# Optimization experiments

Measured on AMD Instinct MI355X. Metric: run time of the kernel, lower is better.

Reference implementation:

```python
import jax, jax.numpy as jnp
import numpy as np

B, N, D_IN, D_OUT, D_EDGE = 2, 512, 128, 128, 32
NEG_SLOPE = 0.2  # GATv2 LeakyReLU default


def _glorot(k, shape):
    lim = np.sqrt(6.0 / (shape[0] + shape[1]))
    return jax.random.uniform(k, shape, jnp.float32, -lim, lim)


def setup_inputs() -> dict:
    key = jax.random.key(0)
    ks = jax.random.split(key, 8)
    return {
        "node_features": jax.random.normal(ks[0], (B, N, D_IN), jnp.float32),
        "adj": jax.random.uniform(ks[1], (B, N, N)) < 0.1,  # sparse-ish dense adjacency
        "edge_features": jax.random.normal(ks[2], (B, N, N, D_EDGE), jnp.float32),
        "mask": jnp.ones((B, N), dtype=bool),
        "W_l": _glorot(ks[3], (D_IN, D_OUT)),   # source (lin_l)
        "b_l": jnp.zeros((D_OUT,), jnp.float32),
        "W_r": _glorot(ks[4], (D_IN, D_OUT)),   # target (lin_r)
        "b_r": jnp.zeros((D_OUT,), jnp.float32),
        "W_e": _glorot(ks[5], (D_EDGE, D_OUT)), # lin_edge (no bias)
        "att": _glorot(ks[6], (1, D_OUT))[0],   # attention vector [D_OUT]
        "bias": jnp.zeros((D_OUT,), jnp.float32),
    }


def _gatv2_dense(x, adj, e, mask, W_l, b_l, W_r, b_r, W_e, att, bias):
    # add self-loops (dense GAT convention)
    adj = adj | jnp.eye(N, dtype=bool)
    x_l = x @ W_l + b_l              # [B,N,D] source transform
    x_r = x @ W_r + b_r              # [B,N,D] target transform
    e_t = e @ W_e                    # [B,N,N,D] edge transform
    # edge (j -> i): pre[b,i,j,:] = x_l[b,j] + x_r[b,i] + e_t[b,i,j]
    pre = x_l[:, None, :, :] + x_r[:, :, None, :] + e_t
    score = jnp.einsum('bijd,d->bij', jax.nn.leaky_relu(pre, NEG_SLOPE), att)
    score = jnp.where(adj, score, -jnp.inf)
    alpha = jax.nn.softmax(score, axis=-1)  # softmax over neighbors j
    out = jnp.einsum('bij,bjd->bid', alpha, x_l) + bias
    return jnp.where(mask[:, :, None], out, 0.0)


def reference(node_features, adj, edge_features, mask, W_l, b_l, W_r, b_r, W_e, att, bias):
    return jax.nn.silu(
        _gatv2_dense(node_features, adj, edge_features, mask,
                     W_l, b_l, W_r, b_r, W_e, att, bias)
    )
```

## Files before the change

### kernel.cpp

```cpp
#include <hip/hip_runtime.h>
#include <math.h>

#define BATCH 2
#define NNODE 512
#define DIN   128
#define DOUT  128
#define DE    32
#define NEG   0.2f
#define TI    4
#define TJ    64
#define TIB   4

typedef __attribute__((ext_vector_type(8))) short bf16x8;
typedef __attribute__((ext_vector_type(4))) float f32x4;

__device__ inline short f2bf(float f) {
    union { float f; unsigned u; } v; v.f = f;
    unsigned r = v.u + 0x7fffu + ((v.u >> 16) & 1u);
    return (short)(r >> 16);
}

template<int CTRL>
__device__ inline float dpp_add(float x) {
    const int y = __builtin_amdgcn_update_dpp(0, __float_as_int(x), CTRL, 0xF, 0xF, false);
    return x + __int_as_float(y);
}
__device__ inline float row16_sum(float x) {
    x = dpp_add<0x128>(x);
    x = dpp_add<0x124>(x);
    x = dpp_add<0x122>(x);
    x = dpp_add<0x121>(x);
    return x;
}

__global__ __launch_bounds__(256) void xlr_kernel(
    const float* __restrict__ x,  const float* __restrict__ Wl,
    const float* __restrict__ bl, const float* __restrict__ Wr,
    const float* __restrict__ br, float* __restrict__ xl,
    float* __restrict__ xr)
{
    const int r0 = blockIdx.x * 4;
    const int d  = threadIdx.x & 127;
    const int hv = threadIdx.x >> 7;
    __shared__ float xs[4][DIN];
    for (int idx = threadIdx.x; idx < 4 * DIN; idx += 256)
        xs[idx >> 7][idx & 127] = x[(size_t)r0 * DIN + idx];
    __syncthreads();
    const int ra = 2 * hv, rb = ra + 1;
    float al0 = bl[d], al1 = al0, ar0 = br[d], ar1 = ar0;
    #pragma unroll 4
    for (int k = 0; k < DIN; ++k) {
        const float wl = Wl[k * DOUT + d], wr = Wr[k * DOUT + d];
        const float xa = xs[ra][k], xb = xs[rb][k];
        al0 = fmaf(xa, wl, al0); al1 = fmaf(xb, wl, al1);
        ar0 = fmaf(xa, wr, ar0); ar1 = fmaf(xb, wr, ar1);
    }
    xl[(size_t)(r0 + ra) * DOUT + d] = al0;
    xl[(size_t)(r0 + rb) * DOUT + d] = al1;
    xr[(size_t)(r0 + ra) * DOUT + d] = ar0;
    xr[(size_t)(r0 + rb) * DOUT + d] = ar1;
}

__global__ __launch_bounds__(256, 4) void score_kernel(
    const float* __restrict__ xl, const float* __restrict__ xr,
    const float* __restrict__ e,  const float* __restrict__ We,
    const float* __restrict__ att, float* __restrict__ sc)
{
    const int bid = blockIdx.x;
    const int jT  = bid & 7;
    const int iT  = (bid >> 3) & 127;
    const int b   = bid >> 10;
    const int i0  = iT * TI, j0 = jT * TJ;
    const int t    = threadIdx.x;
    const int wave = t >> 6;
    const int lane = t & 63;
    const int col  = lane & 15;
    const int g    = lane >> 4;

    __shared__ short WeT_s[DOUT][DE];
    __shared__ float xr_s[TI][DOUT];
    __shared__ float att_s[DOUT];

    for (int idx = t; idx < DE * DOUT; idx += 256) {
        const int k = idx >> 7, d = idx & 127;
        WeT_s[d][k] = f2bf(We[idx]);
    }
    for (int idx = t; idx < TI * DOUT; idx += 256) {
        const int ii = idx >> 7, d = idx & 127;
        xr_s[ii][d] = xr[(size_t)(b * NNODE + i0 + ii) * DOUT + d];
    }
    if (t < DOUT) att_s[t] = att[t];

    f32x4 xlv4[8];
    {
        const float* xb = xl + (size_t)(b * NNODE + j0 + wave * 16 + g * 4) * DOUT + col;
        #pragma unroll
        for (int dt = 0; dt < 8; ++dt)
            #pragma unroll
            for (int r = 0; r < 4; ++r)
                xlv4[dt][r] = xb[(size_t)r * DOUT + dt * 16];
    }
    __syncthreads();

    bf16x8 bf[8];
    float  atv[8];
    #pragma unroll
    for (int dt = 0; dt < 8; ++dt) {
        bf[dt]  = *(const bf16x8*)&WeT_s[dt * 16 + col][g * 8];
        atv[dt] = att_s[dt * 16 + col];
    }

    const int jw = j0 + wave * 16;
    const float* ebase = e + ((size_t)(b * NNODE + i0) * NNODE + jw + col) * DE + g * 8;
    const size_t estep = (size_t)NNODE * DE;

    f32x4 a0 = *(const f32x4*)ebase;
    f32x4 a1 = *(const f32x4*)(ebase + 4);

    for (int i = 0; i < TI; ++i) {
        f32x4 a0n, a1n;
        if (i + 1 < TI) {
            const float* apn = ebase + (size_t)(i + 1) * estep;
            a0n = *(const f32x4*)apn;
            a1n = *(const f32x4*)(apn + 4);
        }
        bf16x8 af;
        af[0] = f2bf(a0[0]); af[1] = f2bf(a0[1]);
        af[2] = f2bf(a0[2]); af[3] = f2bf(a0[3]);
        af[4] = f2bf(a1[0]); af[5] = f2bf(a1[1]);
        af[6] = f2bf(a1[2]); af[7] = f2bf(a1[3]);

        float part[4] = {0.f, 0.f, 0.f, 0.f};
        #pragma unroll
        for (int dt = 0; dt < 8; ++dt) {
            const f32x4 c = __builtin_amdgcn_mfma_f32_16x16x32_bf16(af, bf[dt], xlv4[dt], 0, 0, 0);
            const float xrv = xr_s[i][dt * 16 + col];
            #pragma unroll
            for (int r = 0; r < 4; ++r) {
                float p = c[r] + xrv;
                p = fmaxf(p, NEG * p);
                part[r] = fmaf(atv[dt], p, part[r]);
            }
        }
        #pragma unroll
        for (int r = 0; r < 4; ++r)
            part[r] = row16_sum(part[r]);

        if (col == 0) {
            float4 v;
            float* vp = (float*)&v;
            #pragma unroll
            for (int r = 0; r < 4; ++r) vp[r] = part[r];
            *(float4*)&sc[(size_t)(b * NNODE + i0 + i) * NNODE + jw + g * 4] = v;
        }
        a0 = a0n; a1 = a1n;
    }
}

__global__ __launch_bounds__(256) void agg_kernel(
    const float* __restrict__ xl, const float* __restrict__ sc,
    const void* __restrict__ adjv, const void* __restrict__ maskv,
    const float* __restrict__ bias, float* __restrict__ out)
{
    const int bid = blockIdx.x;
    const int dh  = bid & 1;
    const int iT  = (bid >> 1) & 127;
    const int b   = bid >> 8;
    const int i0  = iT * TIB, d0 = dh * 64;
    const int t    = threadIdx.x;
    const int wave = t >> 6;
    const int lane = t & 63;

    __shared__ float al_s[TIB][NNODE];
    __shared__ float ps_s[4][TIB][64];
    __shared__ float inv_s[TIB];
    __shared__ int   mflag[2];

    if (t < 2) mflag[t] = 0;
    {
        const unsigned* aw = (const unsigned*)adjv;
        unsigned sawF = 0, sawG = 0;
        #pragma unroll
        for (int k = 0; k < 16; ++k) {
            const unsigned w = aw[t + 256 * k];
            sawF |= (w == 0x3f800000u);
            sawG |= (w > 1u);
        }
        if (sawF) atomicOr(&mflag[0], 1);
        if (sawG) atomicOr(&mflag[1], 1);
    }
    for (int idx = t; idx < TIB * NNODE; idx += 256) {
        const int r = idx >> 9, jj = idx & 511;
        al_s[r][jj] = sc[(size_t)(b * NNODE + i0 + r) * NNODE + jj];
    }
    __syncthreads();
    const int byteMode = (!mflag[0] && mflag[1]) ? 1 : 0;

    {
        const int ig = i0 + wave;
        const unsigned char* aB = (const unsigned char*)adjv + (size_t)(b * NNODE + ig) * NNODE;
        const unsigned*      aW = (const unsigned*)adjv + (size_t)(b * NNODE + ig) * NNODE;
        float v[8], m = -1e30f;
        #pragma unroll
        for (int k = 0; k < 8; ++k) {
            const int j = lane + 64 * k;
            const bool conn = (j == ig) ||
                (byteMode ? (aB[j] != 0) : (aW[j] != 0));
            v[k] = conn ? al_s[wave][j] : -1e30f;
            m = fmaxf(m, v[k]);
        }
        #pragma unroll
        for (int off = 32; off; off >>= 1) m = fmaxf(m, __shfl_xor(m, off, 64));
        float s = 0.f;
        #pragma unroll
        for (int k = 0; k < 8; ++k) {
            const float ex = __expf(v[k] - m);
            al_s[wave][lane + 64 * k] = ex;
            s += ex;
        }
        #pragma unroll
        for (int off = 32; off; off >>= 1) s += __shfl_xor(s, off, 64);
        if (lane == 0) inv_s[wave] = 1.f / s;
    }
    __syncthreads();

    const int d = d0 + lane;
    const float* xb = xl + (size_t)b * NNODE * DOUT + d;
    float ac[TIB] = {0.f, 0.f, 0.f, 0.f};
    const int jlo = wave * 128;
    for (int j4 = jlo; j4 < jlo + 128; j4 += 4) {
        const f32x4 a0 = *(const f32x4*)&al_s[0][j4];
        const f32x4 a1 = *(const f32x4*)&al_s[1][j4];
        const f32x4 a2 = *(const f32x4*)&al_s[2][j4];
        const f32x4 a3 = *(const f32x4*)&al_s[3][j4];
        #pragma unroll
        for (int k = 0; k < 4; ++k) {
            const float xv = xb[(size_t)(j4 + k) * DOUT];
            ac[0] = fmaf(a0[k], xv, ac[0]);
            ac[1] = fmaf(a1[k], xv, ac[1]);
            ac[2] = fmaf(a2[k], xv, ac[2]);
            ac[3] = fmaf(a3[k], xv, ac[3]);
        }
    }
    #pragma unroll
    for (int r = 0; r < TIB; ++r) ps_s[wave][r][lane] = ac[r];
    __syncthreads();

    {
        const int r = wave;
        float val = (ps_s[0][r][lane] + ps_s[1][r][lane]) +
                    (ps_s[2][r][lane] + ps_s[3][r][lane]);
        const int mi = b * NNODE + i0 + r;
        const bool mv = byteMode ? (((const unsigned char*)maskv)[mi] != 0)
                                 : (((const unsigned*)maskv)[mi] != 0);
        val = val * inv_s[r] + bias[d];
        if (!mv) val = 0.f;
        val = val / (1.f + __expf(-val));
        out[(size_t)mi * DOUT + d] = val;
    }
}

extern "C" void kernel_launch(void* const* d_in, const int* in_sizes, int n_in,
                              void* d_out, int out_size, void* d_ws, size_t ws_size,
                              hipStream_t stream)
{
    const float* x    = (const float*)d_in[0];
    const void*  adj  = d_in[1];
    const float* e    = (const float*)d_in[2];
    const void*  mask = d_in[3];
    const float* Wl   = (const float*)d_in[4];
    const float* bl   = (const float*)d_in[5];
    const float* Wr   = (const float*)d_in[6];
    const float* br   = (const float*)d_in[7];
    const float* We   = (const float*)d_in[8];
    const float* att  = (const float*)d_in[9];
    const float* bias = (const float*)d_in[10];
    float*       out  = (float*)d_out;

    float* xl = (float*)d_ws;
    float* xr = xl + (size_t)BATCH * NNODE * DOUT;
    float* sc = xr + (size_t)BATCH * NNODE * DOUT;

    xlr_kernel<<<(BATCH * NNODE) / 4, 256, 0, stream>>>(x, Wl, bl, Wr, br, xl, xr);
    score_kernel<<<BATCH * (NNODE / TI) * (NNODE / TJ), 256, 0, stream>>>(
        xl, xr, e, We, att, sc);
    agg_kernel<<<BATCH * (NNODE / TIB) * 2, 256, 0, stream>>>(
        xl, sc, adj, mask, bias, out);
}
```

Measured before the change: 51.43 us.

## Stage edge tiles through LDS with async global_load_lds triple buffering

The score kernel now streams each edge-feature row tile into a swizzled three-slot LDS ring using direct global-to-LDS loads, keeping two rows in flight while the current one is computed. It also doubles the rows per block (TI 4→8), uses packed bf16 conversion instructions, and stages scores in LDS so they leave in coalesced float4 stores. The aim is to hide the memory latency of the dominant 64MB edge tensor read and to cut conversion ALU work. In exchange it adds about 24KB of LDS per block, a barrier per row, and halves the number of blocks, which can lower occupancy.

```diff
diff --git a/kernel.cpp b/kernel.cpp
--- a/kernel.cpp
+++ b/kernel.cpp
@@ -7,7 +7,7 @@
 #define DOUT  128
 #define DE    32
 #define NEG   0.2f
-#define TI    4
+#define TI    8
 #define TJ    64
 #define TIB   4
 
@@ -18,6 +18,19 @@
     union { float f; unsigned u; } v; v.f = f;
     unsigned r = v.u + 0x7fffu + ((v.u >> 16) & 1u);
     return (short)(r >> 16);
+}
+
+__device__ inline unsigned cvtpk(float lo, float hi) {
+    unsigned r;
+    asm("v_cvt_pk_bf16_f32 %0, %1, %2" : "=v"(r) : "v"(lo), "v"(hi));
+    return r;
+}
+typedef union { bf16x8 v; unsigned u[4]; } bfu;
+
+__device__ inline void gload16(const void* g, void* l) {
+    __builtin_amdgcn_global_load_lds(
+        (const __attribute__((address_space(1))) void*)g,
+        (__attribute__((address_space(3))) void*)l, 16, 0, 0);
 }
 
 template<int CTRL>
@@ -61,15 +74,15 @@
     xr[(size_t)(r0 + rb) * DOUT + d] = ar1;
 }
 
-__global__ __launch_bounds__(256, 4) void score_kernel(
+__global__ __launch_bounds__(256, 2) void score_kernel(
     const float* __restrict__ xl, const float* __restrict__ xr,
     const float* __restrict__ e,  const float* __restrict__ We,
     const float* __restrict__ att, float* __restrict__ sc)
 {
     const int bid = blockIdx.x;
     const int jT  = bid & 7;
-    const int iT  = (bid >> 3) & 127;
-    const int b   = bid >> 10;
+    const int iT  = (bid >> 3) & 63;
+    const int b   = bid >> 9;
     const int i0  = iT * TI, j0 = jT * TJ;
     const int t    = threadIdx.x;
     const int wave = t >> 6;
@@ -77,9 +90,11 @@
     const int col  = lane & 15;
     const int g    = lane >> 4;
 
-    __shared__ short WeT_s[DOUT][DE];
-    __shared__ float xr_s[TI][DOUT];
-    __shared__ float att_s[DOUT];
+    __shared__ __align__(16) float ebuf[3][TJ * DE];
+    __shared__ __align__(16) short WeT_s[DOUT][DE];
+    __shared__ __align__(16) float xr_s[TI][DOUT];
+    __shared__ __align__(16) float att_s[DOUT];
+    __shared__ __align__(16) float sc_s[TI][TJ];
 
     for (int idx = t; idx < DE * DOUT; idx += 256) {
         const int k = idx >> 7, d = idx & 127;
@@ -110,30 +125,47 @@
         atv[dt] = att_s[dt * 16 + col];
     }
 
-    const int jw = j0 + wave * 16;
-    const float* ebase = e + ((size_t)(b * NNODE + i0) * NNODE + jw + col) * DE + g * 8;
+    const float* etile = e + ((size_t)(b * NNODE + i0) * NNODE + j0) * DE;
     const size_t estep = (size_t)NNODE * DE;
-
-    f32x4 a0 = *(const f32x4*)ebase;
-    f32x4 a1 = *(const f32x4*)(ebase + 4);
-
+    const unsigned x0  = (unsigned)((wave << 11) + (lane << 4));
+
+    auto STAGE = [&](int s, int i) {
+        const char* gsrc = (const char*)(etile + (size_t)i * estep);
+        #pragma unroll
+        for (int c = 0; c < 2; ++c) {
+            const unsigned x  = x0 + (unsigned)(c << 10);
+            const unsigned sx = x ^ (((x >> 7) & 7u) << 4);
+            gload16(gsrc + sx,
+                    (char*)&ebuf[s][0] + (wave << 11) + (c << 10));
+        }
+    };
+
+    STAGE(0, 0);
+    STAGE(1, 1);
+    asm volatile("s_waitcnt vmcnt(2)" ::: "memory");
+    __builtin_amdgcn_s_barrier();
+    __builtin_amdgcn_sched_barrier(0);
+
+    const int      rrow = wave * 16 + col;
+    const unsigned ys   = ((unsigned)(rrow * 128 + g * 32)) ^
+                          (((unsigned)(rrow & 7)) << 4);
+
+    #pragma unroll
     for (int i = 0; i < TI; ++i) {
-        f32x4 a0n, a1n;
-        if (i + 1 < TI) {
-            const float* apn = ebase + (size_t)(i + 1) * estep;
-            a0n = *(const f32x4*)apn;
-            a1n = *(const f32x4*)(apn + 4);
-        }
-        bf16x8 af;
-        af[0] = f2bf(a0[0]); af[1] = f2bf(a0[1]);
-        af[2] = f2bf(a0[2]); af[3] = f2bf(a0[3]);
-        af[4] = f2bf(a1[0]); af[5] = f2bf(a1[1]);
-        af[6] = f2bf(a1[2]); af[7] = f2bf(a1[3]);
+        if (i + 2 < TI) STAGE((i + 2) % 3, i + 2);
+
+        const char* eb = (const char*)&ebuf[i % 3][0];
+        const f32x4 a0 = *(const f32x4*)(eb + ys);
+        const f32x4 a1 = *(const f32x4*)(eb + (ys ^ 16u));
+
+        bfu af;
+        af.u[0] = cvtpk(a0[0], a0[1]); af.u[1] = cvtpk(a0[2], a0[3]);
+        af.u[2] = cvtpk(a1[0], a1[1]); af.u[3] = cvtpk(a1[2], a1[3]);
 
         float part[4] = {0.f, 0.f, 0.f, 0.f};
         #pragma unroll
         for (int dt = 0; dt < 8; ++dt) {
-            const f32x4 c = __builtin_amdgcn_mfma_f32_16x16x32_bf16(af, bf[dt], xlv4[dt], 0, 0, 0);
+            const f32x4 c = __builtin_amdgcn_mfma_f32_16x16x32_bf16(af.v, bf[dt], xlv4[dt], 0, 0, 0);
             const float xrv = xr_s[i][dt * 16 + col];
             #pragma unroll
             for (int r = 0; r < 4; ++r) {
@@ -143,17 +175,26 @@
             }
         }
         #pragma unroll
-        for (int r = 0; r < 4; ++r)
-            part[r] = row16_sum(part[r]);
+        for (int r = 0; r < 4; ++r) part[r] = row16_sum(part[r]);
 
         if (col == 0) {
-            float4 v;
-            float* vp = (float*)&v;
+            float4 v; float* vp = (float*)&v;
             #pragma unroll
             for (int r = 0; r < 4; ++r) vp[r] = part[r];
-            *(float4*)&sc[(size_t)(b * NNODE + i0 + i) * NNODE + jw + g * 4] = v;
-        }
-        a0 = a0n; a1 = a1n;
+            *(float4*)&sc_s[i][wave * 16 + g * 4] = v;
+        }
+
+        if (i < TI - 2) asm volatile("s_waitcnt vmcnt(2)" ::: "memory");
+        else            asm volatile("s_waitcnt vmcnt(0)" ::: "memory");
+        __builtin_amdgcn_s_barrier();
+        __builtin_amdgcn_sched_barrier(0);
+    }
+
+    __syncthreads();
+    if (t < (TI * TJ) / 4) {
+        const int row = t >> 4, c4 = (t & 15) * 4;
+        *(float4*)&sc[(size_t)(b * NNODE + i0 + row) * NNODE + j0 + c4] =
+            *(const float4*)&sc_s[row][c4];
     }
 }
 
```

After: 51.40 us. Within noise of the previous version (-0.1%).

## Split score kernel d-tiles across waves and use packed bf16 conversion

Applied to the files above, without the earlier changes.

Restructures the score kernel so each block handles 8 target rows by 16 source columns. The four waves each compute two of the eight output d-tiles and combine partial attention sums through shared memory. This lowers register pressure to allow higher occupancy, and swaps the manual float-to-bf16 rounding for the packed hardware convert instruction. In exchange, all four waves load the same edge-feature tile, adding redundant cache traffic, and a shared-memory reduction with an extra barrier is introduced.

```diff
diff --git a/kernel.cpp b/kernel.cpp
--- a/kernel.cpp
+++ b/kernel.cpp
@@ -7,8 +7,7 @@
 #define DOUT  128
 #define DE    32
 #define NEG   0.2f
-#define TI    4
-#define TJ    64
+#define TI    8
 #define TIB   4
 
 typedef __attribute__((ext_vector_type(8))) short bf16x8;
@@ -19,6 +18,13 @@
     unsigned r = v.u + 0x7fffu + ((v.u >> 16) & 1u);
     return (short)(r >> 16);
 }
+
+__device__ inline unsigned cvtpk(float lo, float hi) {
+    unsigned r;
+    asm("v_cvt_pk_bf16_f32 %0, %1, %2" : "=v"(r) : "v"(lo), "v"(hi));
+    return r;
+}
+typedef union { bf16x8 v; unsigned u[4]; } bfu;
 
 template<int CTRL>
 __device__ inline float dpp_add(float x) {
@@ -61,16 +67,16 @@
     xr[(size_t)(r0 + rb) * DOUT + d] = ar1;
 }
 
-__global__ __launch_bounds__(256, 4) void score_kernel(
+__global__ __launch_bounds__(256, 8) void score_kernel(
     const float* __restrict__ xl, const float* __restrict__ xr,
     const float* __restrict__ e,  const float* __restrict__ We,
     const float* __restrict__ att, float* __restrict__ sc)
 {
     const int bid = blockIdx.x;
-    const int jT  = bid & 7;
-    const int iT  = (bid >> 3) & 127;
-    const int b   = bid >> 10;
-    const int i0  = iT * TI, j0 = jT * TJ;
+    const int jT  = bid & 31;
+    const int iT  = (bid >> 5) & 63;
+    const int b   = bid >> 11;
+    const int i0  = iT * TI, j0 = jT * 16;
     const int t    = threadIdx.x;
     const int wave = t >> 6;
     const int lane = t & 63;
@@ -80,6 +86,7 @@
     __shared__ short WeT_s[DOUT][DE];
     __shared__ float xr_s[TI][DOUT];
     __shared__ float att_s[DOUT];
+    __shared__ float ps_s[4][TI][16];
 
     for (int idx = t; idx < DE * DOUT; idx += 256) {
         const int k = idx >> 7, d = idx & 127;
@@ -91,27 +98,25 @@
     }
     if (t < DOUT) att_s[t] = att[t];
 
-    f32x4 xlv4[8];
-    {
-        const float* xb = xl + (size_t)(b * NNODE + j0 + wave * 16 + g * 4) * DOUT + col;
-        #pragma unroll
-        for (int dt = 0; dt < 8; ++dt)
-            #pragma unroll
-            for (int r = 0; r < 4; ++r)
-                xlv4[dt][r] = xb[(size_t)r * DOUT + dt * 16];
-    }
-    __syncthreads();
-
-    bf16x8 bf[8];
-    float  atv[8];
-    #pragma unroll
-    for (int dt = 0; dt < 8; ++dt) {
-        bf[dt]  = *(const bf16x8*)&WeT_s[dt * 16 + col][g * 8];
-        atv[dt] = att_s[dt * 16 + col];
-    }
-
-    const int jw = j0 + wave * 16;
-    const float* ebase = e + ((size_t)(b * NNODE + i0) * NNODE + jw + col) * DE + g * 8;
+    const int dt0 = 2 * wave, dt1 = 2 * wave + 1;
+
+    f32x4 xlc0, xlc1;
+    {
+        const float* xb = xl + (size_t)(b * NNODE + j0 + g * 4) * DOUT + col;
+        #pragma unroll
+        for (int r = 0; r < 4; ++r) {
+            xlc0[r] = xb[(size_t)r * DOUT + dt0 * 16];
+            xlc1[r] = xb[(size_t)r * DOUT + dt1 * 16];
+        }
+    }
+    __syncthreads();
+
+    bf16x8 bf0 = *(const bf16x8*)&WeT_s[dt0 * 16 + col][g * 8];
+    bf16x8 bf1 = *(const bf16x8*)&WeT_s[dt1 * 16 + col][g * 8];
+    const float at0 = att_s[dt0 * 16 + col];
+    const float at1 = att_s[dt1 * 16 + col];
+
+    const float* ebase = e + ((size_t)(b * NNODE + i0) * NNODE + j0 + col) * DE + g * 8;
     const size_t estep = (size_t)NNODE * DE;
 
     f32x4 a0 = *(const f32x4*)ebase;
@@ -124,36 +129,40 @@
             a0n = *(const f32x4*)apn;
             a1n = *(const f32x4*)(apn + 4);
         }
-        bf16x8 af;
-        af[0] = f2bf(a0[0]); af[1] = f2bf(a0[1]);
-        af[2] = f2bf(a0[2]); af[3] = f2bf(a0[3]);
-        af[4] = f2bf(a1[0]); af[5] = f2bf(a1[1]);
-        af[6] = f2bf(a1[2]); af[7] = f2bf(a1[3]);
-
-        float part[4] = {0.f, 0.f, 0.f, 0.f};
-        #pragma unroll
-        for (int dt = 0; dt < 8; ++dt) {
-            const f32x4 c = __builtin_amdgcn_mfma_f32_16x16x32_bf16(af, bf[dt], xlv4[dt], 0, 0, 0);
-            const float xrv = xr_s[i][dt * 16 + col];
+        bfu af;
+        af.u[0] = cvtpk(a0[0], a0[1]); af.u[1] = cvtpk(a0[2], a0[3]);
+        af.u[2] = cvtpk(a1[0], a1[1]); af.u[3] = cvtpk(a1[2], a1[3]);
+
+        const f32x4 c0 = __builtin_amdgcn_mfma_f32_16x16x32_bf16(af.v, bf0, xlc0, 0, 0, 0);
+        const f32x4 c1 = __builtin_amdgcn_mfma_f32_16x16x32_bf16(af.v, bf1, xlc1, 0, 0, 0);
+
+        const float xr0 = xr_s[i][dt0 * 16 + col];
+        const float xr1 = xr_s[i][dt1 * 16 + col];
+        float part[4];
+        #pragma unroll
+        for (int r = 0; r < 4; ++r) {
+            float p = c0[r] + xr0;
+            p = fmaxf(p, NEG * p);
+            float q = c1[r] + xr1;
+            q = fmaxf(q, NEG * q);
+            part[r] = fmaf(at0, p, at1 * q);
+        }
+        #pragma unroll
+        for (int r = 0; r < 4; ++r) part[r] = row16_sum(part[r]);
+
+        if (col == 0) {
             #pragma unroll
-            for (int r = 0; r < 4; ++r) {
-                float p = c[r] + xrv;
-                p = fmaxf(p, NEG * p);
-                part[r] = fmaf(atv[dt], p, part[r]);
-            }
-        }
-        #pragma unroll
-        for (int r = 0; r < 4; ++r)
-            part[r] = row16_sum(part[r]);
-
-        if (col == 0) {
-            float4 v;
-            float* vp = (float*)&v;
-            #pragma unroll
-            for (int r = 0; r < 4; ++r) vp[r] = part[r];
-            *(float4*)&sc[(size_t)(b * NNODE + i0 + i) * NNODE + jw + g * 4] = v;
+            for (int r = 0; r < 4; ++r) ps_s[wave][i][g * 4 + r] = part[r];
         }
         a0 = a0n; a1 = a1n;
+    }
+    __syncthreads();
+
+    if (t < TI * 16) {
+        const int i = t >> 4, jl = t & 15;
+        const float v = (ps_s[0][i][jl] + ps_s[1][i][jl]) +
+                        (ps_s[2][i][jl] + ps_s[3][i][jl]);
+        sc[(size_t)(b * NNODE + i0 + i) * NNODE + j0 + jl] = v;
     }
 }
 
@@ -282,7 +291,7 @@
     float* sc = xr + (size_t)BATCH * NNODE * DOUT;
 
     xlr_kernel<<<(BATCH * NNODE) / 4, 256, 0, stream>>>(x, Wl, bl, Wr, br, xl, xr);
-    score_kernel<<<BATCH * (NNODE / TI) * (NNODE / TJ), 256, 0, stream>>>(
+    score_kernel<<<BATCH * (NNODE / TI) * (NNODE / 16), 256, 0, stream>>>(
         xl, xr, e, We, att, sc);
     agg_kernel<<<BATCH * (NNODE / TIB) * 2, 256, 0, stream>>>(
         xl, sc, adj, mask, bias, out);
```

New measurement: 65.77 us. 27.9% more time.

## Restructure score kernel to one target row per block, looping over source tiles

Applied to the files above, without the earlier changes.

The score kernel now launches one block per (batch, target node i) and loops over eight 64-wide j tiles. Each tile's xl fragments are reloaded from global memory, while xr values stay in registers instead of shared memory. The old i-tile prefetch becomes a prefetch of the next j tile's edge features. The fp32-to-bf16 conversion now uses the packed v_cvt_pk_bf16_f32 instruction, and launch bounds are relaxed to 2 blocks per CU. The grid keeps the same number of blocks (1024) but each block does more serial work, and xl is reloaded per tile, which may raise L2 traffic.

```diff
diff --git a/kernel.cpp b/kernel.cpp
--- a/kernel.cpp
+++ b/kernel.cpp
@@ -7,8 +7,6 @@
 #define DOUT  128
 #define DE    32
 #define NEG   0.2f
-#define TI    4
-#define TJ    64
 #define TIB   4
 
 typedef __attribute__((ext_vector_type(8))) short bf16x8;
@@ -19,6 +17,13 @@
     unsigned r = v.u + 0x7fffu + ((v.u >> 16) & 1u);
     return (short)(r >> 16);
 }
+
+__device__ inline unsigned cvtpk(float lo, float hi) {
+    unsigned r;
+    asm("v_cvt_pk_bf16_f32 %0, %1, %2" : "=v"(r) : "v"(lo), "v"(hi));
+    return r;
+}
+typedef union { bf16x8 v; unsigned u[4]; } bfu;
 
 template<int CTRL>
 __device__ inline float dpp_add(float x) {
@@ -61,16 +66,13 @@
     xr[(size_t)(r0 + rb) * DOUT + d] = ar1;
 }
 
-__global__ __launch_bounds__(256, 4) void score_kernel(
+__global__ __launch_bounds__(256, 2) void score_kernel(
     const float* __restrict__ xl, const float* __restrict__ xr,
     const float* __restrict__ e,  const float* __restrict__ We,
     const float* __restrict__ att, float* __restrict__ sc)
 {
-    const int bid = blockIdx.x;
-    const int jT  = bid & 7;
-    const int iT  = (bid >> 3) & 127;
-    const int b   = bid >> 10;
-    const int i0  = iT * TI, j0 = jT * TJ;
+    const int bi   = blockIdx.x;
+    const int b    = bi >> 9;
     const int t    = threadIdx.x;
     const int wave = t >> 6;
     const int lane = t & 63;
@@ -78,82 +80,70 @@
     const int g    = lane >> 4;
 
     __shared__ short WeT_s[DOUT][DE];
-    __shared__ float xr_s[TI][DOUT];
     __shared__ float att_s[DOUT];
 
     for (int idx = t; idx < DE * DOUT; idx += 256) {
         const int k = idx >> 7, d = idx & 127;
         WeT_s[d][k] = f2bf(We[idx]);
     }
-    for (int idx = t; idx < TI * DOUT; idx += 256) {
-        const int ii = idx >> 7, d = idx & 127;
-        xr_s[ii][d] = xr[(size_t)(b * NNODE + i0 + ii) * DOUT + d];
-    }
     if (t < DOUT) att_s[t] = att[t];
-
-    f32x4 xlv4[8];
-    {
-        const float* xb = xl + (size_t)(b * NNODE + j0 + wave * 16 + g * 4) * DOUT + col;
-        #pragma unroll
-        for (int dt = 0; dt < 8; ++dt)
-            #pragma unroll
-            for (int r = 0; r < 4; ++r)
-                xlv4[dt][r] = xb[(size_t)r * DOUT + dt * 16];
-    }
     __syncthreads();
 
     bf16x8 bf[8];
-    float  atv[8];
+    float  atv[8], xrv[8];
     #pragma unroll
     for (int dt = 0; dt < 8; ++dt) {
         bf[dt]  = *(const bf16x8*)&WeT_s[dt * 16 + col][g * 8];
         atv[dt] = att_s[dt * 16 + col];
-    }
-
-    const int jw = j0 + wave * 16;
-    const float* ebase = e + ((size_t)(b * NNODE + i0) * NNODE + jw + col) * DE + g * 8;
-    const size_t estep = (size_t)NNODE * DE;
-
-    f32x4 a0 = *(const f32x4*)ebase;
-    f32x4 a1 = *(const f32x4*)(ebase + 4);
-
-    for (int i = 0; i < TI; ++i) {
-        f32x4 a0n, a1n;
-        if (i + 1 < TI) {
-            const float* apn = ebase + (size_t)(i + 1) * estep;
-            a0n = *(const f32x4*)apn;
-            a1n = *(const f32x4*)(apn + 4);
-        }
-        bf16x8 af;
-        af[0] = f2bf(a0[0]); af[1] = f2bf(a0[1]);
-        af[2] = f2bf(a0[2]); af[3] = f2bf(a0[3]);
-        af[4] = f2bf(a1[0]); af[5] = f2bf(a1[1]);
-        af[6] = f2bf(a1[2]); af[7] = f2bf(a1[3]);
+        xrv[dt] = xr[(size_t)bi * DOUT + dt * 16 + col];
+    }
+
+    const float* ew = e + ((size_t)bi * NNODE + wave * 16 + col) * DE + g * 8;
+    const size_t pstep = 64 * DE;
+    const float* xlb = xl + (size_t)(b * NNODE + wave * 16 + g * 4) * DOUT + col;
+
+    f32x4 a0 = *(const f32x4*)ew;
+    f32x4 a1 = *(const f32x4*)(ew + 4);
+
+    for (int s = 0; s < 8; ++s) {
+        const int spf = (s + 1 < 8) ? s + 1 : s;
+        const float* apn = ew + (size_t)spf * pstep;
+        const f32x4 n0 = *(const f32x4*)apn;
+        const f32x4 n1 = *(const f32x4*)(apn + 4);
+
+        const float* xp = xlb + (size_t)s * 64 * DOUT;
+        f32x4 xlv4[8];
+        #pragma unroll
+        for (int dt = 0; dt < 8; ++dt)
+            #pragma unroll
+            for (int r = 0; r < 4; ++r)
+                xlv4[dt][r] = xp[(size_t)r * DOUT + dt * 16];
+
+        bfu af;
+        af.u[0] = cvtpk(a0[0], a0[1]); af.u[1] = cvtpk(a0[2], a0[3]);
+        af.u[2] = cvtpk(a1[0], a1[1]); af.u[3] = cvtpk(a1[2], a1[3]);
 
         float part[4] = {0.f, 0.f, 0.f, 0.f};
         #pragma unroll
         for (int dt = 0; dt < 8; ++dt) {
-            const f32x4 c = __builtin_amdgcn_mfma_f32_16x16x32_bf16(af, bf[dt], xlv4[dt], 0, 0, 0);
-            const float xrv = xr_s[i][dt * 16 + col];
+            const f32x4 c = __builtin_amdgcn_mfma_f32_16x16x32_bf16(af.v, bf[dt], xlv4[dt], 0, 0, 0);
             #pragma unroll
             for (int r = 0; r < 4; ++r) {
-                float p = c[r] + xrv;
+                float p = c[r] + xrv[dt];
                 p = fmaxf(p, NEG * p);
                 part[r] = fmaf(atv[dt], p, part[r]);
             }
         }
         #pragma unroll
-        for (int r = 0; r < 4; ++r)
-            part[r] = row16_sum(part[r]);
+        for (int r = 0; r < 4; ++r) part[r] = row16_sum(part[r]);
 
         if (col == 0) {
-            float4 v;
-            float* vp = (float*)&v;
+            float4 v; float* vp = (float*)&v;
             #pragma unroll
             for (int r = 0; r < 4; ++r) vp[r] = part[r];
-            *(float4*)&sc[(size_t)(b * NNODE + i0 + i) * NNODE + jw + g * 4] = v;
-        }
-        a0 = a0n; a1 = a1n;
+            *(float4*)&sc[(size_t)bi * NNODE + s * 64 + wave * 16 + g * 4] = v;
+        }
+        a0 = n0; a1 = n1;
     }
 }
 
@@ -282,8 +272,7 @@
     float* sc = xr + (size_t)BATCH * NNODE * DOUT;
 
     xlr_kernel<<<(BATCH * NNODE) / 4, 256, 0, stream>>>(x, Wl, bl, Wr, br, xl, xr);
-    score_kernel<<<BATCH * (NNODE / TI) * (NNODE / TJ), 256, 0, stream>>>(
-        xl, xr, e, We, att, sc);
+    score_kernel<<<BATCH * NNODE, 256, 0, stream>>>(xl, xr, e, We, att, sc);
     agg_kernel<<<BATCH * (NNODE / TIB) * 2, 256, 0, stream>>>(
         xl, sc, adj, mask, bias, out);
 }
```

Result: no change. 50.72 us (-1.4%).
